# Kernel optimization log

Hardware: AMD Instinct MI355X
Metric: run time of the kernel (lower is better)

## Reference

```python
import jax, jax.numpy as jnp
import numpy as np

N = 50000
E = 800000
F_IN = 256
C = 64  # embedding_size, heads=1
EDGE_DIM = 2
NEG_SLOPE = 0.01


def setup_inputs() -> dict:
    key = jax.random.key(0)
    ks = jax.random.split(key, 12)
    s = 1.0 / np.sqrt(C)
    return {
        "x": jax.random.normal(ks[0], (N, F_IN), jnp.float32),
        "edge_index": jax.random.randint(ks[1], (2, E), 0, N, jnp.int64),
        "edge_attr": jax.random.normal(ks[2], (E, EDGE_DIM), jnp.float32),
        "Wf": jax.random.normal(ks[3], (F_IN, C), jnp.float32) / np.sqrt(F_IN),
        "bf": jnp.zeros((C,), jnp.float32),
        "Wq": jax.random.normal(ks[4], (C, C), jnp.float32) * s,
        "bq": jnp.zeros((C,), jnp.float32),
        "Wk": jax.random.normal(ks[5], (C, C), jnp.float32) * s,
        "bk": jnp.zeros((C,), jnp.float32),
        "Wv": jax.random.normal(ks[6], (C, C), jnp.float32) * s,
        "bv": jnp.zeros((C,), jnp.float32),
        "We": jax.random.normal(ks[7], (EDGE_DIM, C), jnp.float32) / np.sqrt(EDGE_DIM),
        "Wskip": jax.random.normal(ks[8], (C, C), jnp.float32) * s,
        "bskip": jnp.zeros((C,), jnp.float32),
    }


def reference(x, edge_index, edge_attr, Wf, bf, Wq, bq, Wk, bk, Wv, bv, We, Wskip, bskip):
    n = x.shape[0]
    src, dst = edge_index[0], edge_index[1]
    inv_sqrt_c = 1.0 / np.sqrt(C)

    h = jax.nn.leaky_relu(x @ Wf + bf, NEG_SLOPE)
    e = edge_attr @ We  # [E, C] edge embedding (lin_edge, no bias), same each layer

    for _ in range(3):
        q = h @ Wq + bq
        k = h @ Wk + bk
        v = h @ Wv + bv
        kj = k[src] + e                                  # [E, C] key + edge feat
        alpha = jnp.sum(q[dst] * kj, axis=-1) * inv_sqrt_c  # [E]
        # per-destination softmax
        m = jax.ops.segment_max(alpha, dst, num_segments=n)
        ex = jnp.exp(alpha - m[dst])
        den = jax.ops.segment_sum(ex, dst, num_segments=n)
        a = ex / den[dst]                                # [E]
        msg = (v[src] + e) * a[:, None]                  # [E, C]
        agg = jax.ops.segment_sum(msg, dst, num_segments=n)  # [N, C]
        h = jax.nn.leaky_relu(agg + h @ Wskip + bskip, NEG_SLOPE)  # root_weight skip
    return h
```

## Files before the change

### kernel.cpp

```cpp
#include <hip/hip_runtime.h>
#include <hip/hip_fp16.h>

#define NN 50000
#define NE 800000
#define FIN 256
#define C 64
#define NEG_SLOPE 0.01f
#define SCAN_BLOCKS ((NN + 255) / 256)
#define CSR_CHUNKS (NE / 256)

typedef float f32x16 __attribute__((ext_vector_type(16)));

__device__ __forceinline__ float leaky(float v) { return v > 0.f ? v : NEG_SLOPE * v; }

__global__ __launch_bounds__(256) void k_tw(const float* __restrict__ Wq,
                                            const float* __restrict__ Wk,
                                            const float* __restrict__ Wv,
                                            const float* __restrict__ Ws,
                                            float* __restrict__ Wt) {
    const int idx = blockIdx.x * 256 + threadIdx.x;
    if (idx >= 4 * 64 * 64) return;
    const int m = idx >> 12, r = idx & 4095, c = r >> 6, k = r & 63;
    const float* W = (m == 0) ? Wq : (m == 1) ? Wk : (m == 2) ? Wv : Ws;
    Wt[idx] = W[k * 64 + c];
}

__global__ __launch_bounds__(256) void k_feat(const float* __restrict__ x,
                                              const float* __restrict__ Wf,
                                              const float* __restrict__ bf,
                                              float* __restrict__ h) {
    __shared__ float4 Sx[64][33];
    const int t = threadIdx.x;
    const int lane = t & 63;
    const int q = __builtin_amdgcn_readfirstlane(t) >> 6;
    const int base = blockIdx.x * 64;

    const float4* x4 = (const float4*)x;
    float4 acc[4];
#pragma unroll
    for (int cp = 0; cp < 4; ++cp) acc[cp] = make_float4(0.f, 0.f, 0.f, 0.f);

#define FRAG(wreg, xs)                                                      \
    acc[0].x = fmaf(xs, wreg[0],  acc[0].x);                                \
    acc[0].y = fmaf(xs, wreg[1],  acc[0].y);                                \
    acc[0].z = fmaf(xs, wreg[2],  acc[0].z);                                \
    acc[0].w = fmaf(xs, wreg[3],  acc[0].w);                                \
    acc[1].x = fmaf(xs, wreg[4],  acc[1].x);                                \
    acc[1].y = fmaf(xs, wreg[5],  acc[1].y);                                \
    acc[1].z = fmaf(xs, wreg[6],  acc[1].z);                                \
    acc[1].w = fmaf(xs, wreg[7],  acc[1].w);                                \
    acc[2].x = fmaf(xs, wreg[8],  acc[2].x);                                \
    acc[2].y = fmaf(xs, wreg[9],  acc[2].y);                                \
    acc[2].z = fmaf(xs, wreg[10], acc[2].z);                                \
    acc[2].w = fmaf(xs, wreg[11], acc[2].w);                                \
    acc[3].x = fmaf(xs, wreg[12], acc[3].x);                                \
    acc[3].y = fmaf(xs, wreg[13], acc[3].y);                                \
    acc[3].z = fmaf(xs, wreg[14], acc[3].z);                                \
    acc[3].w = fmaf(xs, wreg[15], acc[3].w);

    for (int ph = 0; ph < 2; ++ph) {
#pragma unroll
        for (int i = 0; i < 8; ++i) {
            const int idx = t + i * 256;
            const int row = idx >> 5, c = idx & 31;
            int nn = base + row; if (nn >= NN) nn = NN - 1;
            Sx[row][c] = x4[(size_t)nn * 64 + ph * 32 + c];
        }
        __syncthreads();

        const float* wbase = Wf + (size_t)(ph * 128) * 64 + q * 16;
#pragma unroll
        for (int j = 0; j < 32; ++j) {
            const float4 xv = Sx[lane][j];
            const float* wrow = wbase + (size_t)j * 256;
            f32x16 w0_, w1_, w2_, w3_;
            asm volatile("s_load_dwordx16 %0, %4, 0x0\n\t"
                         "s_load_dwordx16 %1, %4, 0x100\n\t"
                         "s_load_dwordx16 %2, %4, 0x200\n\t"
                         "s_load_dwordx16 %3, %4, 0x300\n\t"
                         "s_waitcnt lgkmcnt(0)"
                         : "=&s"(w0_), "=&s"(w1_), "=&s"(w2_), "=&s"(w3_)
                         : "s"(wrow));
            FRAG(w0_, xv.x)
            FRAG(w1_, xv.y)
            FRAG(w2_, xv.z)
            FRAG(w3_, xv.w)
        }
        __syncthreads();
    }
#undef FRAG

    float4* O = (float4*)Sx;
    const float4* bf4 = (const float4*)bf;
#pragma unroll
    for (int cp = 0; cp < 4; ++cp) {
        const float4 b = bf4[q * 4 + cp];
        float4 r;
        r.x = leaky(acc[cp].x + b.x); r.y = leaky(acc[cp].y + b.y);
        r.z = leaky(acc[cp].z + b.z); r.w = leaky(acc[cp].w + b.w);
        O[lane * 17 + q * 4 + cp] = r;
    }
    __syncthreads();
#pragma unroll
    for (int i = 0; i < 4; ++i) {
        const int idx = t + i * 256;
        const int row = idx >> 4, c = idx & 15;
        const int nn = base + row;
        if (nn < NN) ((float4*)h)[(size_t)nn * 16 + c] = O[row * 17 + c];
    }
}

#define QKVS_NPB 32

__global__ __launch_bounds__(256) void k_qkvs(const float* __restrict__ h,
                                              const float* __restrict__ Wt,
                                              const float* __restrict__ bq,
                                              const float* __restrict__ bk,
                                              const float* __restrict__ bv,
                                              const float* __restrict__ bs,
                                              float* __restrict__ qkvs) {
    const int t = threadIdx.x;
    const int lane = t & 63;
    const int sec = __builtin_amdgcn_readfirstlane(t) >> 6;
    const int base = blockIdx.x * QKVS_NPB;

    int m, cidx;
    float bias;
    if (sec == 0)      { m = 0; cidx = lane; bias = bq[lane]; }
    else if (sec == 1) { m = 3; cidx = lane; bias = bs[lane]; }
    else {
        cidx = ((sec - 2) << 5) + (lane >> 1);
        m = 1 + (lane & 1);
        bias = (lane & 1) ? bv[cidx] : bk[cidx];
    }

    const float4* wb = (const float4*)(Wt + ((size_t)m << 12) + ((size_t)cidx << 6));
    float4 w[16];
#pragma unroll
    for (int j = 0; j < 16; ++j) w[j] = wb[j];

    const int nmax = (base + QKVS_NPB <= NN) ? QKVS_NPB : (NN - base);
    for (int i = 0; i < nmax; ++i) {
        const float* hrow = h + (size_t)(base + i) * 64;
        f32x16 ha, hb, hc, hd;
        asm volatile("s_load_dwordx16 %0, %4, 0x0\n\t"
                     "s_load_dwordx16 %1, %4, 0x40\n\t"
                     "s_load_dwordx16 %2, %4, 0x80\n\t"
                     "s_load_dwordx16 %3, %4, 0xc0\n\t"
                     "s_waitcnt lgkmcnt(0)"
                     : "=&s"(ha), "=&s"(hb), "=&s"(hc), "=&s"(hd)
                     : "s"(hrow));
        float a0 = 0.f, a1 = 0.f, a2 = 0.f, a3 = 0.f;
#pragma unroll
        for (int j = 0; j < 4; ++j) {
            a0 = fmaf(ha[4 * j + 0], w[j].x, a0);
            a1 = fmaf(ha[4 * j + 1], w[j].y, a1);
            a2 = fmaf(ha[4 * j + 2], w[j].z, a2);
            a3 = fmaf(ha[4 * j + 3], w[j].w, a3);
        }
#pragma unroll
        for (int j = 0; j < 4; ++j) {
            a0 = fmaf(hb[4 * j + 0], w[4 + j].x, a0);
            a1 = fmaf(hb[4 * j + 1], w[4 + j].y, a1);
            a2 = fmaf(hb[4 * j + 2], w[4 + j].z, a2);
            a3 = fmaf(hb[4 * j + 3], w[4 + j].w, a3);
        }
#pragma unroll
        for (int j = 0; j < 4; ++j) {
            a0 = fmaf(hc[4 * j + 0], w[8 + j].x, a0);
            a1 = fmaf(hc[4 * j + 1], w[8 + j].y, a1);
            a2 = fmaf(hc[4 * j + 2], w[8 + j].z, a2);
            a3 = fmaf(hc[4 * j + 3], w[8 + j].w, a3);
        }
#pragma unroll
        for (int j = 0; j < 4; ++j) {
            a0 = fmaf(hd[4 * j + 0], w[12 + j].x, a0);
            a1 = fmaf(hd[4 * j + 1], w[12 + j].y, a1);
            a2 = fmaf(hd[4 * j + 2], w[12 + j].z, a2);
            a3 = fmaf(hd[4 * j + 3], w[12 + j].w, a3);
        }
        const float val = ((a0 + a1) + (a2 + a3)) + bias;
        float* orow = qkvs + (size_t)(base + i) * 192;
        if (sec == 0) {
            orow[lane] = val;
        } else if (sec == 1) {
            orow[128 + lane] = val;
        } else {
            __half* kvh = (__half*)(orow + 64);
            kvh[((sec - 2) << 6) + lane] = __float2half(val);
        }
    }
}

__global__ __launch_bounds__(256) void k_hist(const int* __restrict__ ei,
                                              int* __restrict__ deg) {
    const int e = blockIdx.x * 256 + threadIdx.x;
    if (e >= NE) return;
    atomicAdd(&deg[ei[NE + e]], 1);
}

__global__ __launch_bounds__(256) void k_blocksum(const int* __restrict__ deg,
                                                  int* __restrict__ bsum) {
    __shared__ int sh[256];
    const int t = threadIdx.x;
    const int idx = blockIdx.x * 256 + t;
    sh[t] = (idx < NN) ? deg[idx] : 0;
    __syncthreads();
#pragma unroll
    for (int off = 128; off > 0; off >>= 1) {
        if (t < off) sh[t] += sh[t + off];
        __syncthreads();
    }
    if (t == 0) bsum[blockIdx.x] = sh[0];
}

__global__ __launch_bounds__(256) void k_scanb(const int* __restrict__ bsum,
                                               int* __restrict__ boff) {
    __shared__ int sh[256];
    const int t = threadIdx.x;
    const int v = (t < SCAN_BLOCKS) ? bsum[t] : 0;
    sh[t] = v;
    __syncthreads();
#pragma unroll
    for (int off = 1; off < 256; off <<= 1) {
        const int x = (t >= off) ? sh[t - off] : 0;
        __syncthreads();
        sh[t] += x;
        __syncthreads();
    }
    if (t < SCAN_BLOCKS) boff[t] = sh[t] - v;
}

__global__ __launch_bounds__(256) void k_writeptr(const int* __restrict__ deg,
                                                  const int* __restrict__ boff,
                                                  int* __restrict__ row_ptr,
                                                  int* __restrict__ cursor) {
    __shared__ int sh[256];
    const int t = threadIdx.x;
    const int idx = blockIdx.x * 256 + t;
    const int v = (idx < NN) ? deg[idx] : 0;
    sh[t] = v;
    __syncthreads();
#pragma unroll
    for (int off = 1; off < 256; off <<= 1) {
        const int x = (t >= off) ? sh[t - off] : 0;
        __syncthreads();
        sh[t] += x;
        __syncthreads();
    }
    if (idx < NN) {
        const int r = boff[blockIdx.x] + sh[t] - v;
        row_ptr[idx] = r;
        cursor[idx] = r;
    }
    if (idx == 0) row_ptr[NN] = NE;
}

__global__ __launch_bounds__(256) void k_csr(const int* __restrict__ ei,
                                             const float* __restrict__ eattr,
                                             const int* __restrict__ row_ptr,
                                             int* __restrict__ cursor,
                                             uint2* __restrict__ erec) {
    const int chunk = blockIdx.x >> 3;
    const unsigned myx = blockIdx.x & 7;
    const int e = chunk * 256 + threadIdx.x;
    const int dst = ei[NE + e];
    const int rp = row_ptr[dst];
    const unsigned owner = (unsigned)rp / (NE / 8u);
    if (owner != myx) return;
    const int pos = atomicAdd(&cursor[dst], 1);
    const __half2 a = __floats2half2_rn(eattr[e * 2], eattr[e * 2 + 1]);
    erec[pos] = make_uint2((unsigned)ei[e], *(const unsigned*)&a);
}

__global__ __launch_bounds__(256) void k_conv(const int* __restrict__ row_ptr,
                                              const uint2* __restrict__ erec,
                                              const float* __restrict__ We,
                                              const float* __restrict__ qkvs,
                                              float* __restrict__ hout) {
    const int t = threadIdx.x;
    const int lane = t & 63;
    const int g = lane >> 4;
    const int p = lane & 15;
    const int wv = __builtin_amdgcn_readfirstlane(t) >> 6;
    const int d = blockIdx.x * 4 + wv;
    if (d >= NN) return;

    const float* qrow = qkvs + (size_t)d * 192;
    const float4 q4  = *(const float4*)(qrow + 4 * p);
    const float4 w0  = *(const float4*)(We + 4 * p);
    const float4 w1  = *(const float4*)(We + 64 + 4 * p);

    float pg0 = q4.x * w0.x + q4.y * w0.y + q4.z * w0.z + q4.w * w0.w;
    float pg1 = q4.x * w1.x + q4.y * w1.y + q4.z * w1.z + q4.w * w1.w;
#pragma unroll
    for (int mask = 1; mask <= 8; mask <<= 1) {
        pg0 += __shfl_xor(pg0, mask);
        pg1 += __shfl_xor(pg1, mask);
    }
    const float g0 = pg0, g1 = pg1;

    const int i0 = row_ptr[d], i1 = row_ptr[d + 1];
    const char* kvbase = (const char*)qkvs + 256 + ((size_t)p << 4);

    float m = -1e30f, l = 0.f, S1 = 0.f, S2 = 0.f;
    float4 acc = make_float4(0.f, 0.f, 0.f, 0.f);

#pragma unroll 2
    for (int i = i0 + g; i < i1; i += 4) {
        const uint2 r = erec[i];
        const __half2 ah = *(const __half2*)&r.y;
        const float a0 = __low2float(ah), a1 = __high2float(ah);
        const float4 kvl = *(const float4*)(kvbase + (size_t)r.x * 768);
        const __half2* hv = (const __half2*)&kvl;
        const float kf0 = __low2float(hv[0]), vf0 = __high2float(hv[0]);
        const float kf1 = __low2float(hv[1]), vf1 = __high2float(hv[1]);
        const float kf2 = __low2float(hv[2]), vf2 = __high2float(hv[2]);
        const float kf3 = __low2float(hv[3]), vf3 = __high2float(hv[3]);
        float dot = q4.x * kf0 + q4.y * kf1 + q4.z * kf2 + q4.w * kf3;
        dot += __shfl_xor(dot, 1);
        dot += __shfl_xor(dot, 2);
        dot += __shfl_xor(dot, 4);
        dot += __shfl_xor(dot, 8);
        const float P = (dot + g0 * a0 + g1 * a1) * 0.125f;
        const float mn = fmaxf(m, P);
        const float s = __expf(m - mn);
        const float e = __expf(P - mn);
        l = l * s + e;
        acc.x = acc.x * s + vf0 * e;
        acc.y = acc.y * s + vf1 * e;
        acc.z = acc.z * s + vf2 * e;
        acc.w = acc.w * s + vf3 * e;
        S1 = S1 * s + a0 * e;
        S2 = S2 * s + a1 * e;
        m = mn;
    }

#pragma unroll
    for (int mask = 16; mask <= 32; mask <<= 1) {
        const float mo  = __shfl_xor(m, mask);
        const float lo  = __shfl_xor(l, mask);
        const float axo = __shfl_xor(acc.x, mask);
        const float ayo = __shfl_xor(acc.y, mask);
        const float azo = __shfl_xor(acc.z, mask);
        const float awo = __shfl_xor(acc.w, mask);
        const float S1o = __shfl_xor(S1, mask);
        const float S2o = __shfl_xor(S2, mask);
        const float mn = fmaxf(m, mo);
        const float sA = __expf(m - mn);
        const float sB = __expf(mo - mn);
        l     = l * sA + lo * sB;
        acc.x = acc.x * sA + axo * sB;
        acc.y = acc.y * sA + ayo * sB;
        acc.z = acc.z * sA + azo * sB;
        acc.w = acc.w * sA + awo * sB;
        S1    = S1 * sA + S1o * sB;
        S2    = S2 * sA + S2o * sB;
        m = mn;
    }

    if (lane < 16) {
        const float inv = (l > 0.f) ? 1.f / l : 0.f;
        const float4 sk = *(const float4*)(qrow + 128 + 4 * p);
        float4 r;
        r.x = leaky((acc.x + S1 * w0.x + S2 * w1.x) * inv + sk.x);
        r.y = leaky((acc.y + S1 * w0.y + S2 * w1.y) * inv + sk.y);
        r.z = leaky((acc.z + S1 * w0.z + S2 * w1.z) * inv + sk.z);
        r.w = leaky((acc.w + S1 * w0.w + S2 * w1.w) * inv + sk.w);
        *(float4*)(hout + (size_t)d * C + 4 * p) = r;
    }
}

extern "C" void kernel_launch(void* const* d_in, const int* in_sizes, int n_in,
                              void* d_out, int out_size, void* d_ws, size_t ws_size,
                              hipStream_t stream) {
    const float* x     = (const float*)d_in[0];
    const int*   ei    = (const int*)d_in[1];
    const float* eattr = (const float*)d_in[2];
    const float* Wf    = (const float*)d_in[3];
    const float* bf    = (const float*)d_in[4];
    const float* Wq    = (const float*)d_in[5];
    const float* bq    = (const float*)d_in[6];
    const float* Wk    = (const float*)d_in[7];
    const float* bk    = (const float*)d_in[8];
    const float* Wv    = (const float*)d_in[9];
    const float* bv    = (const float*)d_in[10];
    const float* We    = (const float*)d_in[11];
    const float* Ws    = (const float*)d_in[12];
    const float* bs    = (const float*)d_in[13];
    float* out = (float*)d_out;

    char* p = (char*)d_ws;
    float*  h       = (float*)p;  p += (size_t)NN * C * 4;
    float*  qkvs    = (float*)p;  p += (size_t)NN * 192 * 4;
    float*  Wt      = (float*)p;  p += (size_t)4 * 64 * 64 * 4;
    int*    deg     = (int*)p;    p += (size_t)NN * 4;
    int*    row_ptr = (int*)p;    p += (size_t)(NN + 1) * 4;
    int*    cursor  = (int*)p;    p += (size_t)NN * 4;
    int*    bsum    = (int*)p;    p += (size_t)SCAN_BLOCKS * 4;
    int*    boff    = (int*)p;    p += (size_t)SCAN_BLOCKS * 4;
    uint2*  erec    = (uint2*)p;  p += (size_t)NE * 8;

    k_tw<<<64, 256, 0, stream>>>(Wq, Wk, Wv, Ws, Wt);
    hipMemsetAsync(deg, 0, (size_t)NN * 4, stream);
    k_hist<<<CSR_CHUNKS, 256, 0, stream>>>(ei, deg);
    k_blocksum<<<SCAN_BLOCKS, 256, 0, stream>>>(deg, bsum);
    k_scanb<<<1, 256, 0, stream>>>(bsum, boff);
    k_writeptr<<<SCAN_BLOCKS, 256, 0, stream>>>(deg, boff, row_ptr, cursor);
    k_csr<<<CSR_CHUNKS * 8, 256, 0, stream>>>(ei, eattr, row_ptr, cursor, erec);

    const int feat_grid = (NN + 63) / 64;
    const int qkvs_grid = (NN + QKVS_NPB - 1) / QKVS_NPB;

    k_feat<<<feat_grid, 256, 0, stream>>>(x, Wf, bf, h);

    for (int layer = 0; layer < 3; ++layer) {
        k_qkvs<<<qkvs_grid, 256, 0, stream>>>(h, Wt, bq, bk, bv, bs, qkvs);
        float* hout = (layer == 2) ? out : h;
        k_conv<<<(NN + 3) / 4, 256, 0, stream>>>(row_ptr, erec, We, qkvs, hout);
    }
}
```

Baseline: 482.6 us.

## Build CSR via two-level bucket sort and process two edges per conv iteration

```diff
diff --git a/kernel.cpp b/kernel.cpp
--- a/kernel.cpp
+++ b/kernel.cpp
@@ -7,7 +7,10 @@
 #define C 64
 #define NEG_SLOPE 0.01f
 #define SCAN_BLOCKS ((NN + 255) / 256)
-#define CSR_CHUNKS (NE / 256)
+#define NBUCK 196
+#define BCAP 8192
+#define EB_CHUNK 2048
+#define EB_BLOCKS ((NE + EB_CHUNK - 1) / EB_CHUNK)
 
 typedef float f32x16 __attribute__((ext_vector_type(16)));
 
@@ -192,11 +195,63 @@
     }
 }
 
-__global__ __launch_bounds__(256) void k_hist(const int* __restrict__ ei,
-                                              int* __restrict__ deg) {
-    const int e = blockIdx.x * 256 + threadIdx.x;
-    if (e >= NE) return;
-    atomicAdd(&deg[ei[NE + e]], 1);
+__global__ __launch_bounds__(256) void k_bucket(const int* __restrict__ ei,
+                                                const float* __restrict__ eattr,
+                                                int* __restrict__ gcur,
+                                                uint2* __restrict__ ebuck) {
+    __shared__ int hist[NBUCK], lbase[NBUCK], lcur[NBUCK];
+    const int t = threadIdx.x;
+    const int base = blockIdx.x * EB_CHUNK;
+    if (t < NBUCK) { hist[t] = 0; lcur[t] = 0; }
+    __syncthreads();
+
+    int dcache[8];
+#pragma unroll
+    for (int i = 0; i < 8; ++i) {
+        const int e = base + i * 256 + t;
+        int d = -1;
+        if (e < NE) {
+            d = ei[NE + e];
+            atomicAdd(&hist[d >> 8], 1);
+        }
+        dcache[i] = d;
+    }
+    __syncthreads();
+    if (t < NBUCK && hist[t] > 0)
+        lbase[t] = atomicAdd(&gcur[t], hist[t]);
+    __syncthreads();
+
+#pragma unroll
+    for (int i = 0; i < 8; ++i) {
+        const int e = base + i * 256 + t;
+        const int d = dcache[i];
+        if (d >= 0) {
+            const int b = d >> 8;
+            const int rank = atomicAdd(&lcur[b], 1);
+            const __half2 a = __floats2half2_rn(eattr[e * 2], eattr[e * 2 + 1]);
+            const unsigned src = (unsigned)ei[e];
+            ebuck[(size_t)b * BCAP + lbase[b] + rank] =
+                make_uint2(((unsigned)d << 16) | src, *(const unsigned*)&a);
+        }
+    }
+}
+
+__global__ __launch_bounds__(256) void k_fin_deg(const int* __restrict__ gcur,
+                                                 const uint2* __restrict__ ebuck,
+                                                 int* __restrict__ deg) {
+    __shared__ int dcnt[256];
+    const int t = threadIdx.x;
+    const int b = blockIdx.x;
+    dcnt[t] = 0;
+    __syncthreads();
+    const int n = gcur[b];
+    for (int i = t; i < n; i += 256) {
+        const unsigned x = ebuck[(size_t)b * BCAP + i].x;
+        atomicAdd(&dcnt[(x >> 16) & 255], 1);
+    }
+    __syncthreads();
+    const int idx = b * 256 + t;
+    if (idx < NN) deg[idx] = dcnt[t];
 }
 
 __global__ __launch_bounds__(256) void k_blocksum(const int* __restrict__ deg,
@@ -233,8 +288,7 @@
 
 __global__ __launch_bounds__(256) void k_writeptr(const int* __restrict__ deg,
                                                   const int* __restrict__ boff,
-                                                  int* __restrict__ row_ptr,
-                                                  int* __restrict__ cursor) {
+                                                  int* __restrict__ row_ptr) {
     __shared__ int sh[256];
     const int t = threadIdx.x;
     const int idx = blockIdx.x * 256 + t;
@@ -248,29 +302,27 @@
         sh[t] += x;
         __syncthreads();
     }
-    if (idx < NN) {
-        const int r = boff[blockIdx.x] + sh[t] - v;
-        row_ptr[idx] = r;
-        cursor[idx] = r;
-    }
+    if (idx < NN) row_ptr[idx] = boff[blockIdx.x] + sh[t] - v;
     if (idx == 0) row_ptr[NN] = NE;
 }
 
-__global__ __launch_bounds__(256) void k_csr(const int* __restrict__ ei,
-                                             const float* __restrict__ eattr,
-                                             const int* __restrict__ row_ptr,
-                                             int* __restrict__ cursor,
-                                             uint2* __restrict__ erec) {
-    const int chunk = blockIdx.x >> 3;
-    const unsigned myx = blockIdx.x & 7;
-    const int e = chunk * 256 + threadIdx.x;
-    const int dst = ei[NE + e];
-    const int rp = row_ptr[dst];
-    const unsigned owner = (unsigned)rp / (NE / 8u);
-    if (owner != myx) return;
-    const int pos = atomicAdd(&cursor[dst], 1);
-    const __half2 a = __floats2half2_rn(eattr[e * 2], eattr[e * 2 + 1]);
-    erec[pos] = make_uint2((unsigned)ei[e], *(const unsigned*)&a);
+__global__ __launch_bounds__(256) void k_fin_scat(const int* __restrict__ gcur,
+                                                  const uint2* __restrict__ ebuck,
+                                                  const int* __restrict__ row_ptr,
+                                                  uint2* __restrict__ erec) {
+    __shared__ int pcur[256];
+    const int t = threadIdx.x;
+    const int b = blockIdx.x;
+    const int idx = b * 256 + t;
+    pcur[t] = (idx < NN) ? row_ptr[idx] : 0;
+    __syncthreads();
+    const int n = gcur[b];
+    for (int i = t; i < n; i += 256) {
+        const uint2 rec = ebuck[(size_t)b * BCAP + i];
+        const int d = (rec.x >> 16) & 255;
+        const int pos = atomicAdd(&pcur[d], 1);
+        erec[pos] = make_uint2(rec.x & 0xFFFFu, rec.y);
+    }
 }
 
 __global__ __launch_bounds__(256) void k_conv(const int* __restrict__ row_ptr,
@@ -306,8 +358,48 @@
     float m = -1e30f, l = 0.f, S1 = 0.f, S2 = 0.f;
     float4 acc = make_float4(0.f, 0.f, 0.f, 0.f);
 
-#pragma unroll 2
-    for (int i = i0 + g; i < i1; i += 4) {
+    int i = i0 + g;
+    for (; i + 4 < i1; i += 8) {
+        const uint2 ra = erec[i];
+        const uint2 rb = erec[i + 4];
+        const __half2 aha = *(const __half2*)&ra.y;
+        const __half2 ahb = *(const __half2*)&rb.y;
+        const float a0a = __low2float(aha), a1a = __high2float(aha);
+        const float a0b = __low2float(ahb), a1b = __high2float(ahb);
+        const float4 kva = *(const float4*)(kvbase + (size_t)ra.x * 768);
+        const float4 kvb = *(const float4*)(kvbase + (size_t)rb.x * 768);
+        const __half2* ha = (const __half2*)&kva;
+        const __half2* hb = (const __half2*)&kvb;
+        const float ka0 = __low2float(ha[0]), va0 = __high2float(ha[0]);
+        const float ka1 = __low2float(ha[1]), va1 = __high2float(ha[1]);
+        const float ka2 = __low2float(ha[2]), va2 = __high2float(ha[2]);
+        const float ka3 = __low2float(ha[3]), va3 = __high2float(ha[3]);
+        const float kb0 = __low2float(hb[0]), vb0 = __high2float(hb[0]);
+        const float kb1 = __low2float(hb[1]), vb1 = __high2float(hb[1]);
+        const float kb2 = __low2float(hb[2]), vb2 = __high2float(hb[2]);
+        const float kb3 = __low2float(hb[3]), vb3 = __high2float(hb[3]);
+        float da = q4.x * ka0 + q4.y * ka1 + q4.z * ka2 + q4.w * ka3;
+        float db = q4.x * kb0 + q4.y * kb1 + q4.z * kb2 + q4.w * kb3;
+        da += __shfl_xor(da, 1);  db += __shfl_xor(db, 1);
+        da += __shfl_xor(da, 2);  db += __shfl_xor(db, 2);
+        da += __shfl_xor(da, 4);  db += __shfl_xor(db, 4);
+        da += __shfl_xor(da, 8);  db += __shfl_xor(db, 8);
+        const float Pa = (da + g0 * a0a + g1 * a1a) * 0.125f;
+        const float Pb = (db + g0 * a0b + g1 * a1b) * 0.125f;
+        const float mn = fmaxf(m, fmaxf(Pa, Pb));
+        const float s  = __expf(m - mn);
+        const float ea = __expf(Pa - mn);
+        const float eb = __expf(Pb - mn);
+        l = l * s + ea + eb;
+        acc.x = acc.x * s + va0 * ea + vb0 * eb;
+        acc.y = acc.y * s + va1 * ea + vb1 * eb;
+        acc.z = acc.z * s + va2 * ea + vb2 * eb;
+        acc.w = acc.w * s + va3 * ea + vb3 * eb;
+        S1 = S1 * s + a0a * ea + a0b * eb;
+        S2 = S2 * s + a1a * ea + a1b * eb;
+        m = mn;
+    }
+    for (; i < i1; i += 4) {
         const uint2 r = erec[i];
         const __half2 ah = *(const __half2*)&r.y;
         const float a0 = __low2float(ah), a1 = __high2float(ah);
@@ -396,18 +488,20 @@
     float*  Wt      = (float*)p;  p += (size_t)4 * 64 * 64 * 4;
     int*    deg     = (int*)p;    p += (size_t)NN * 4;
     int*    row_ptr = (int*)p;    p += (size_t)(NN + 1) * 4;
-    int*    cursor  = (int*)p;    p += (size_t)NN * 4;
     int*    bsum    = (int*)p;    p += (size_t)SCAN_BLOCKS * 4;
     int*    boff    = (int*)p;    p += (size_t)SCAN_BLOCKS * 4;
+    int*    gcur    = (int*)p;    p += (size_t)NBUCK * 4;
     uint2*  erec    = (uint2*)p;  p += (size_t)NE * 8;
+    uint2*  ebuck   = (uint2*)p;  p += (size_t)NBUCK * BCAP * 8;
 
     k_tw<<<64, 256, 0, stream>>>(Wq, Wk, Wv, Ws, Wt);
-    hipMemsetAsync(deg, 0, (size_t)NN * 4, stream);
-    k_hist<<<CSR_CHUNKS, 256, 0, stream>>>(ei, deg);
+    hipMemsetAsync(gcur, 0, (size_t)NBUCK * 4, stream);
+    k_bucket<<<EB_BLOCKS, 256, 0, stream>>>(ei, eattr, gcur, ebuck);
+    k_fin_deg<<<NBUCK, 256, 0, stream>>>(gcur, ebuck, deg);
     k_blocksum<<<SCAN_BLOCKS, 256, 0, stream>>>(deg, bsum);
     k_scanb<<<1, 256, 0, stream>>>(bsum, boff);
-    k_writeptr<<<SCAN_BLOCKS, 256, 0, stream>>>(deg, boff, row_ptr, cursor);
-    k_csr<<<CSR_CHUNKS * 8, 256, 0, stream>>>(ei, eattr, row_ptr, cursor, erec);
+    k_writeptr<<<SCAN_BLOCKS, 256, 0, stream>>>(deg, boff, row_ptr);
+    k_fin_scat<<<NBUCK, 256, 0, stream>>>(gcur, ebuck, row_ptr, erec);
 
     const int feat_grid = (NN + 63) / 64;
     const int qkvs_grid = (NN + QKVS_NPB - 1) / QKVS_NPB;
```

After: 426.4 us. 11.7% less time.
